# Performance work log

Hardware: AMD Instinct MI355X
Metric: run time of the kernel (lower is better)

## Reference

```python
import jax, jax.numpy as jnp
import numpy as np

B, T, D_MODEL, N_HEADS = 2, 2048, 4096, 32
D_HEAD = D_MODEL // N_HEADS
ROPE_THETA = 20000.0


def _rope_tables(seq_len, d_head, theta):
    # Faithful to RotaryEmbedding + apply_rotary_emb's `[..., ::2]` slicing:
    # emb = concat(freqs, freqs) along feature dim, then every-other element taken.
    inv_freq = 1.0 / (theta ** (jnp.arange(0, d_head, 2, dtype=jnp.float32) / d_head))  # [d/2]
    t = jnp.arange(seq_len, dtype=jnp.float32)
    freqs = jnp.einsum('i,j->ij', t, inv_freq)          # [T, d/2]
    emb = jnp.concatenate([freqs, freqs], axis=-1)       # [T, d]
    cos_h = jnp.cos(emb)[:, ::2]                         # [T, d/2]
    sin_h = jnp.sin(emb)[:, ::2]                         # [T, d/2]
    return cos_h, sin_h


def _apply_rope(x, cos_h, sin_h):
    # x: [B, H, T, d]; pairs are interleaved (even/odd feature indices).
    x1 = x[..., 0::2]
    x2 = x[..., 1::2]
    r1 = x1 * cos_h - x2 * sin_h
    r2 = x1 * sin_h + x2 * cos_h
    return jnp.stack((r1, r2), axis=-1).reshape(x.shape)


def setup_inputs() -> dict:
    key = jax.random.key(0)
    kx, kq, kk, kv, ko = jax.random.split(key, 5)
    s = 0.02
    return {
        'hidden_states': jax.random.normal(kx, (B, T, D_MODEL), dtype=jnp.float32),
        'Wq': jax.random.normal(kq, (D_MODEL, D_MODEL), dtype=jnp.float32) * s,
        'Wk': jax.random.normal(kk, (D_MODEL, D_MODEL), dtype=jnp.float32) * s,
        'Wv': jax.random.normal(kv, (D_MODEL, D_MODEL), dtype=jnp.float32) * s,
        'Wo': jax.random.normal(ko, (D_MODEL, D_MODEL), dtype=jnp.float32) * s,
    }


def reference(hidden_states, Wq, Wk, Wv, Wo):
    Bs, Ts, C = hidden_states.shape
    H, Dh = N_HEADS, C // N_HEADS

    # QKV projections (nn.Linear: y = x @ W.T), split heads -> [B, H, T, Dh]
    def proj(W):
        return (hidden_states @ W.T).reshape(Bs, Ts, H, Dh).transpose(0, 2, 1, 3)

    q, k, v = proj(Wq), proj(Wk), proj(Wv)

    cos_h, sin_h = _rope_tables(Ts, Dh, ROPE_THETA)
    q = _apply_rope(q, cos_h, sin_h)
    k = _apply_rope(k, cos_h, sin_h)

    # Causal scaled-dot-product attention (flash path semantics)
    scale = 1.0 / jnp.sqrt(jnp.asarray(Dh, dtype=q.dtype))
    scores = jnp.einsum('bhqd,bhkd->bhqk', q, k) * scale      # [B,H,T,T]
    causal = jnp.tril(jnp.ones((Ts, Ts), dtype=bool))
    scores = jnp.where(causal, scores, jnp.finfo(scores.dtype).min)
    probs = jax.nn.softmax(scores, axis=-1)
    attn = jnp.einsum('bhqk,bhkd->bhqd', probs, v)            # [B,H,T,Dh]

    attn = attn.transpose(0, 2, 1, 3).reshape(Bs, Ts, C)
    return attn @ Wo.T
```

## Files before the change

kernel.cpp:

```cpp
#include <hip/hip_runtime.h>
#include <hip/hip_bf16.h>


typedef __bf16 bf16x8 __attribute__((ext_vector_type(8)));
typedef __bf16 bf16x4 __attribute__((ext_vector_type(4)));
typedef float  f32x4  __attribute__((ext_vector_type(4)));

#define GLD_A1(p) ((__attribute__((address_space(1))) void*)(p))
#define GLD_A3(p) ((__attribute__((address_space(3))) void*)(p))

static constexpr int   BATCH = 2;
static constexpr int   TSEQ  = 2048;
static constexpr int   DM    = 4096;
static constexpr int   NH    = 32;
static constexpr int   DH    = 128;
static constexpr size_t TS   = (size_t)DM * DM;

__global__ __launch_bounds__(256) void cast_f32_bf16(const float* __restrict__ in,
                                                     __bf16* __restrict__ out) {
    size_t id = (size_t)blockIdx.x * blockDim.x + threadIdx.x;
    float4 v = ((const float4*)in)[id];
    bf16x4 o = { (__bf16)v.x, (__bf16)v.y, (__bf16)v.z, (__bf16)v.w };
    *(bf16x4*)(out + id * 4) = o;
}

template <bool OUT_F32>
__global__ __launch_bounds__(256) void gemm_nt(const __bf16* __restrict__ A,
                                               const __bf16* __restrict__ W,
                                               void* __restrict__ Cout) {
    constexpr int Kd = 4096, Nd = 4096;
    __shared__ alignas(16) __bf16 As[128 * 32];
    __shared__ alignas(16) __bf16 Bs[128 * 32];

    const int t = threadIdx.x, w = t >> 6, L = t & 63;
    const int lane15 = L & 15, quad = L >> 4;
    const int rowBlock = blockIdx.y * 128, colBlock = blockIdx.x * 128;
    const int wr = (w >> 1) * 64, wc = (w & 1) * 64;

    f32x4 acc[4][4] = {};

    for (int kb = 0; kb < Kd; kb += 32) {
        __syncthreads();
#pragma unroll
        for (int i = 0; i < 2; i++) {
            const int chunk = w * 128 + i * 64 + L;
            const int row = chunk >> 2, c8 = (chunk & 3) * 8;
            __builtin_amdgcn_global_load_lds(
                GLD_A1(A + (size_t)(rowBlock + row) * Kd + kb + c8),
                GLD_A3(As + (size_t)(w * 128 + i * 64) * 8), 16, 0, 0);
            __builtin_amdgcn_global_load_lds(
                GLD_A1(W + (size_t)(colBlock + row) * Kd + kb + c8),
                GLD_A3(Bs + (size_t)(w * 128 + i * 64) * 8), 16, 0, 0);
        }
        __syncthreads();

        bf16x8 a[4], b[4];
#pragma unroll
        for (int i = 0; i < 4; i++)
            a[i] = *(const bf16x8*)(As + (wr + i * 16 + lane15) * 32 + quad * 8);
#pragma unroll
        for (int j = 0; j < 4; j++)
            b[j] = *(const bf16x8*)(Bs + (wc + j * 16 + lane15) * 32 + quad * 8);
#pragma unroll
        for (int i = 0; i < 4; i++)
#pragma unroll
            for (int j = 0; j < 4; j++)
                acc[i][j] = __builtin_amdgcn_mfma_f32_16x16x32_bf16(a[i], b[j], acc[i][j], 0, 0, 0);
    }

#pragma unroll
    for (int i = 0; i < 4; i++)
#pragma unroll
        for (int j = 0; j < 4; j++)
#pragma unroll
            for (int r = 0; r < 4; r++) {
                const size_t gm = rowBlock + wr + i * 16 + quad * 4 + r;
                const size_t gn = colBlock + wc + j * 16 + lane15;
                if (OUT_F32)
                    ((float*)Cout)[gm * Nd + gn] = acc[i][j][r];
                else
                    ((__bf16*)Cout)[gm * Nd + gn] = (__bf16)acc[i][j][r];
            }
}

__global__ __launch_bounds__(256) void rope_inplace(__bf16* __restrict__ X) {
    const size_t id = (size_t)blockIdx.x * blockDim.x + threadIdx.x;
    const int g = (int)(id & 511);
    const size_t row = id >> 9;
    const int tpos = (int)(row & (TSEQ - 1));
    __bf16* p = X + row * DM + (size_t)g * 8;
    bf16x8 v = *(const bf16x8*)p;
    bf16x8 o;
#pragma unroll
    for (int pr = 0; pr < 4; pr++) {
        const int pcol = g * 4 + pr;
        const int j = (2 * (pcol & 63)) & 63;
        const float inv = exp2f(-(float)j * (14.287712379549449f / 64.0f));
        const float ang = (float)tpos * inv;
        float s, c;
        sincosf(ang, &s, &c);
        const float x0 = (float)v[2 * pr], x1 = (float)v[2 * pr + 1];
        o[2 * pr]     = (__bf16)(x0 * c - x1 * s);
        o[2 * pr + 1] = (__bf16)(x0 * s + x1 * c);
    }
    *(bf16x8*)p = o;
}

__global__ __launch_bounds__(256) void flash_attn(const __bf16* __restrict__ Qg,
                                                  const __bf16* __restrict__ Kg,
                                                  const __bf16* __restrict__ Vg,
                                                  __bf16* __restrict__ Og) {
    const int qb = blockIdx.x;
    const int bh = blockIdx.y;
    const int b = bh >> 5, h = bh & 31;
    const size_t base = (size_t)b * TSEQ * DM + (size_t)h * DH;
    const __bf16* Qp = Qg + base;
    const __bf16* Kp = Kg + base;
    const __bf16* Vp = Vg + base;
    __bf16*       Op = Og + base;

    __shared__ alignas(16) __bf16 Ks[64 * 128];
    __shared__ alignas(16) __bf16 Vt[128 * 64];
    __shared__ alignas(16) __bf16 Ps[64 * 72];

    const int t = threadIdx.x, w = t >> 6, L = t & 63;
    const int lane15 = L & 15, quad = L >> 4;
    const int sw = (lane15 & 7) << 4;

    bf16x8 aq[4];
    {
        const int qrow = qb * 64 + w * 16 + lane15;
#pragma unroll
        for (int ks = 0; ks < 4; ++ks)
            aq[ks] = *(const bf16x8*)(Qp + (size_t)qrow * DM + ks * 32 + quad * 8);
    }

    f32x4 o[8] = {};
    float m_i[4], l_i[4];
#pragma unroll
    for (int r = 0; r < 4; r++) { m_i[r] = -1e30f; l_i[r] = 0.0f; }
    const float scale = 0.08838834764831845f;

    for (int kt = 0; kt <= qb; ++kt) {
        bf16x8 vv[4];
#pragma unroll
        for (int c = 0; c < 4; c++) {
            const int d0 = (c * 4 + w) * 8;
            vv[c] = *(const bf16x8*)(Vp + (size_t)(kt * 64 + L) * DM + d0);
        }
#pragma unroll
        for (int c = 0; c < 4; c++) {
            const int chunk0 = c * 256 + (w << 6);
            const int chunk  = chunk0 + L;
            const int row = chunk >> 4;
            const int ssw = (chunk & 15) ^ (row & 7);
            __builtin_amdgcn_global_load_lds(
                GLD_A1(Kp + (size_t)(kt * 64 + row) * DM + ssw * 8),
                GLD_A3((char*)Ks + chunk0 * 16), 16, 0, 0);
        }
#pragma unroll
        for (int c = 0; c < 4; c++) {
            const int d0 = (c * 4 + w) * 8;
#pragma unroll
            for (int jj = 0; jj < 8; jj++)
                *(__bf16*)((char*)Vt + (d0 + jj) * 128 + ((L * 2) ^ (jj << 4))) = vv[c][jj];
        }
        __syncthreads();

        f32x4 s[4] = {};
        __builtin_amdgcn_s_setprio(1);
#pragma unroll
        for (int ks = 0; ks < 4; ++ks)
#pragma unroll
            for (int n = 0; n < 4; n++) {
                bf16x8 bk = *(const bf16x8*)((const char*)Ks + (n * 16 + lane15) * 256
                                             + ((ks * 64 + quad * 16) ^ sw));
                s[n] = __builtin_amdgcn_mfma_f32_16x16x32_bf16(aq[ks], bk, s[n], 0, 0, 0);
            }
        __builtin_amdgcn_s_setprio(0);

        const bool diag = (kt == qb);
#pragma unroll
        for (int n = 0; n < 4; n++) {
            const int col = kt * 64 + n * 16 + lane15;
#pragma unroll
            for (int r = 0; r < 4; r++) {
                const int rowq = qb * 64 + w * 16 + quad * 4 + r;
                float sv = s[n][r] * scale;
                if (diag && col > rowq) sv = -1e30f;
                s[n][r] = sv;
            }
        }

        float mx[4], al[4], rs[4];
#pragma unroll
        for (int r = 0; r < 4; r++)
            mx[r] = fmaxf(fmaxf(s[0][r], s[1][r]), fmaxf(s[2][r], s[3][r]));
#pragma unroll
        for (int off = 8; off >= 1; off >>= 1)
#pragma unroll
            for (int r = 0; r < 4; r++)
                mx[r] = fmaxf(mx[r], __shfl_xor(mx[r], off));
#pragma unroll
        for (int r = 0; r < 4; r++) {
            const float mn = fmaxf(m_i[r], mx[r]);
            al[r] = __expf(m_i[r] - mn);
            m_i[r] = mn;
            rs[r] = 0.0f;
        }
#pragma unroll
        for (int n = 0; n < 4; n++)
#pragma unroll
            for (int r = 0; r < 4; r++) {
                const float p = __expf(s[n][r] - m_i[r]);
                rs[r] += p;
                Ps[(w * 16 + quad * 4 + r) * 72 + n * 16 + lane15] = (__bf16)p;
            }
#pragma unroll
        for (int off = 8; off >= 1; off >>= 1)
#pragma unroll
            for (int r = 0; r < 4; r++)
                rs[r] += __shfl_xor(rs[r], off);
#pragma unroll
        for (int r = 0; r < 4; r++) l_i[r] = l_i[r] * al[r] + rs[r];
#pragma unroll
        for (int d = 0; d < 8; ++d)
#pragma unroll
            for (int r = 0; r < 4; r++) o[d][r] *= al[r];

        __syncthreads();

        __builtin_amdgcn_s_setprio(1);
#pragma unroll
        for (int ks2 = 0; ks2 < 2; ++ks2) {
            bf16x8 ap = *(const bf16x8*)(Ps + (w * 16 + lane15) * 72 + ks2 * 32 + quad * 8);
#pragma unroll
            for (int d = 0; d < 8; ++d) {
                bf16x8 bv = *(const bf16x8*)((const char*)Vt + (d * 16 + lane15) * 128
                                             + ((ks2 * 64 + quad * 16) ^ sw));
                o[d] = __builtin_amdgcn_mfma_f32_16x16x32_bf16(ap, bv, o[d], 0, 0, 0);
            }
        }
        __builtin_amdgcn_s_setprio(0);
        __syncthreads();
    }

    float inv_l[4];
#pragma unroll
    for (int r = 0; r < 4; r++) inv_l[r] = 1.0f / l_i[r];
#pragma unroll
    for (int d = 0; d < 8; ++d)
#pragma unroll
        for (int r = 0; r < 4; r++) {
            const int rowq = qb * 64 + w * 16 + quad * 4 + r;
            Op[(size_t)rowq * DM + d * 16 + lane15] = (__bf16)(o[d][r] * inv_l[r]);
        }
}

extern "C" void kernel_launch(void* const* d_in, const int* in_sizes, int n_in,
                              void* d_out, int out_size, void* d_ws, size_t ws_size,
                              hipStream_t stream) {
    const float* hs = (const float*)d_in[0];
    const float* Wq = (const float*)d_in[1];
    const float* Wk = (const float*)d_in[2];
    const float* Wv = (const float*)d_in[3];
    const float* Wo = (const float*)d_in[4];
    float* out = (float*)d_out;

    __bf16* hs_b = (__bf16*)d_ws;
    __bf16* wq_b = hs_b + TS;
    __bf16* wk_b = wq_b + TS;
    __bf16* wv_b = wk_b + TS;
    __bf16* wo_b = wv_b + TS;
    __bf16* Qb   = wo_b + TS;
    __bf16* Kb   = Qb + TS;
    __bf16* Vb   = Kb + TS;
    __bf16* Ab   = Vb + TS;
    if (ws_size < 9 * TS * sizeof(__bf16)) return;

    const dim3 blk(256);
    const int castGrid = (int)(TS / 4 / 256);
    cast_f32_bf16<<<castGrid, blk, 0, stream>>>(hs, hs_b);
    cast_f32_bf16<<<castGrid, blk, 0, stream>>>(Wq, wq_b);
    cast_f32_bf16<<<castGrid, blk, 0, stream>>>(Wk, wk_b);
    cast_f32_bf16<<<castGrid, blk, 0, stream>>>(Wv, wv_b);
    cast_f32_bf16<<<castGrid, blk, 0, stream>>>(Wo, wo_b);

    const dim3 ggrid(32, 32);
    gemm_nt<false><<<ggrid, blk, 0, stream>>>(hs_b, wq_b, (void*)Qb);
    gemm_nt<false><<<ggrid, blk, 0, stream>>>(hs_b, wk_b, (void*)Kb);
    gemm_nt<false><<<ggrid, blk, 0, stream>>>(hs_b, wv_b, (void*)Vb);

    const int ropeGrid = (int)(TS / 8 / 256);
    rope_inplace<<<ropeGrid, blk, 0, stream>>>(Qb);
    rope_inplace<<<ropeGrid, blk, 0, stream>>>(Kb);

    flash_attn<<<dim3(32, 64), blk, 0, stream>>>(Qb, Kb, Vb, Ab);

    gemm_nt<true><<<ggrid, blk, 0, stream>>>(Ab, wo_b, (void*)out);
}
```

Baseline: 1.507 ms.

## Transpose flash-attention S layout, reverse block order, and batch cast/rope launches

```diff
diff --git a/kernel.cpp b/kernel.cpp
--- a/kernel.cpp
+++ b/kernel.cpp
@@ -4,6 +4,7 @@
 
 typedef __bf16 bf16x8 __attribute__((ext_vector_type(8)));
 typedef __bf16 bf16x4 __attribute__((ext_vector_type(4)));
+typedef __bf16 bf16x2 __attribute__((ext_vector_type(2)));
 typedef float  f32x4  __attribute__((ext_vector_type(4)));
 
 #define GLD_A1(p) ((__attribute__((address_space(1))) void*)(p))
@@ -16,12 +17,19 @@
 static constexpr int   DH    = 128;
 static constexpr size_t TS   = (size_t)DM * DM;
 
-__global__ __launch_bounds__(256) void cast_f32_bf16(const float* __restrict__ in,
-                                                     __bf16* __restrict__ out) {
+__global__ __launch_bounds__(256) void cast5_f32_bf16(const float* __restrict__ s0,
+                                                      const float* __restrict__ s1,
+                                                      const float* __restrict__ s2,
+                                                      const float* __restrict__ s3,
+                                                      const float* __restrict__ s4,
+                                                      __bf16* __restrict__ out) {
+    const int which = blockIdx.y;
+    const float* s = which == 0 ? s0 : which == 1 ? s1 : which == 2 ? s2
+                   : which == 3 ? s3 : s4;
     size_t id = (size_t)blockIdx.x * blockDim.x + threadIdx.x;
-    float4 v = ((const float4*)in)[id];
+    float4 v = ((const float4*)s)[id];
     bf16x4 o = { (__bf16)v.x, (__bf16)v.y, (__bf16)v.z, (__bf16)v.w };
-    *(bf16x4*)(out + id * 4) = o;
+    *(bf16x4*)(out + (size_t)which * TS + id * 4) = o;
 }
 
 template <bool OUT_F32>
@@ -83,7 +91,9 @@
             }
 }
 
-__global__ __launch_bounds__(256) void rope_inplace(__bf16* __restrict__ X) {
+__global__ __launch_bounds__(256) void rope2_inplace(__bf16* __restrict__ Q,
+                                                     __bf16* __restrict__ K) {
+    __bf16* X = blockIdx.y == 0 ? Q : K;
     const size_t id = (size_t)blockIdx.x * blockDim.x + threadIdx.x;
     const int g = (int)(id & 511);
     const size_t row = id >> 9;
@@ -110,7 +120,7 @@
                                                   const __bf16* __restrict__ Kg,
                                                   const __bf16* __restrict__ Vg,
                                                   __bf16* __restrict__ Og) {
-    const int qb = blockIdx.x;
+    const int qb = 31 - blockIdx.x;
     const int bh = blockIdx.y;
     const int b = bh >> 5, h = bh & 31;
     const size_t base = (size_t)b * TSEQ * DM + (size_t)h * DH;
@@ -121,27 +131,26 @@
 
     __shared__ alignas(16) __bf16 Ks[64 * 128];
     __shared__ alignas(16) __bf16 Vt[128 * 64];
-    __shared__ alignas(16) __bf16 Ps[64 * 72];
+    __shared__ alignas(16) __bf16 Ps[64 * 64];
 
     const int t = threadIdx.x, w = t >> 6, L = t & 63;
     const int lane15 = L & 15, quad = L >> 4;
     const int sw = (lane15 & 7) << 4;
-
-    bf16x8 aq[4];
-    {
-        const int qrow = qb * 64 + w * 16 + lane15;
-#pragma unroll
-        for (int ks = 0; ks < 4; ++ks)
-            aq[ks] = *(const bf16x8*)(Qp + (size_t)qrow * DM + ks * 32 + quad * 8);
-    }
+    const int rowPs = w * 16 + lane15;
+
+    bf16x8 bq[4];
+    const int qrow = qb * 64 + w * 16 + lane15;
+#pragma unroll
+    for (int ks = 0; ks < 4; ++ks)
+        bq[ks] = *(const bf16x8*)(Qp + (size_t)qrow * DM + ks * 32 + quad * 8);
 
     f32x4 o[8] = {};
-    float m_i[4], l_i[4];
-#pragma unroll
-    for (int r = 0; r < 4; r++) { m_i[r] = -1e30f; l_i[r] = 0.0f; }
+    float m_i = -1e30f, l_i = 0.0f;
     const float scale = 0.08838834764831845f;
 
     for (int kt = 0; kt <= qb; ++kt) {
+        if (kt) __syncthreads();
+
         bf16x8 vv[4];
 #pragma unroll
         for (int c = 0; c < 4; c++) {
@@ -173,67 +182,72 @@
         for (int ks = 0; ks < 4; ++ks)
 #pragma unroll
             for (int n = 0; n < 4; n++) {
-                bf16x8 bk = *(const bf16x8*)((const char*)Ks + (n * 16 + lane15) * 256
+                bf16x8 ak = *(const bf16x8*)((const char*)Ks + (n * 16 + lane15) * 256
                                              + ((ks * 64 + quad * 16) ^ sw));
-                s[n] = __builtin_amdgcn_mfma_f32_16x16x32_bf16(aq[ks], bk, s[n], 0, 0, 0);
+                s[n] = __builtin_amdgcn_mfma_f32_16x16x32_bf16(ak, bq[ks], s[n], 0, 0, 0);
             }
         __builtin_amdgcn_s_setprio(0);
 
         const bool diag = (kt == qb);
 #pragma unroll
-        for (int n = 0; n < 4; n++) {
-            const int col = kt * 64 + n * 16 + lane15;
+        for (int n = 0; n < 4; n++)
 #pragma unroll
             for (int r = 0; r < 4; r++) {
-                const int rowq = qb * 64 + w * 16 + quad * 4 + r;
+                const int col = kt * 64 + n * 16 + quad * 4 + r;
                 float sv = s[n][r] * scale;
-                if (diag && col > rowq) sv = -1e30f;
+                if (diag && col > qrow) sv = -1e30f;
                 s[n][r] = sv;
             }
-        }
-
-        float mx[4], al[4], rs[4];
-#pragma unroll
-        for (int r = 0; r < 4; r++)
-            mx[r] = fmaxf(fmaxf(s[0][r], s[1][r]), fmaxf(s[2][r], s[3][r]));
-#pragma unroll
-        for (int off = 8; off >= 1; off >>= 1)
-#pragma unroll
-            for (int r = 0; r < 4; r++)
-                mx[r] = fmaxf(mx[r], __shfl_xor(mx[r], off));
-#pragma unroll
-        for (int r = 0; r < 4; r++) {
-            const float mn = fmaxf(m_i[r], mx[r]);
-            al[r] = __expf(m_i[r] - mn);
-            m_i[r] = mn;
-            rs[r] = 0.0f;
-        }
+
+        float mx = s[0][0];
 #pragma unroll
         for (int n = 0; n < 4; n++)
 #pragma unroll
+            for (int r = 0; r < 4; r++) mx = fmaxf(mx, s[n][r]);
+        mx = fmaxf(mx, __shfl_xor(mx, 16));
+        mx = fmaxf(mx, __shfl_xor(mx, 32));
+        const float mn = fmaxf(m_i, mx);
+        const float al = __expf(m_i - mn);
+        m_i = mn;
+
+        float p[4][4];
+        float rs = 0.0f;
+#pragma unroll
+        for (int n = 0; n < 4; n++)
+#pragma unroll
             for (int r = 0; r < 4; r++) {
-                const float p = __expf(s[n][r] - m_i[r]);
-                rs[r] += p;
-                Ps[(w * 16 + quad * 4 + r) * 72 + n * 16 + lane15] = (__bf16)p;
-            }
-#pragma unroll
-        for (int off = 8; off >= 1; off >>= 1)
-#pragma unroll
-            for (int r = 0; r < 4; r++)
-                rs[r] += __shfl_xor(rs[r], off);
-#pragma unroll
-        for (int r = 0; r < 4; r++) l_i[r] = l_i[r] * al[r] + rs[r];
+                p[n][r] = __expf(s[n][r] - mn);
+                rs += p[n][r];
+            }
+        rs += __shfl_xor(rs, 16);
+        rs += __shfl_xor(rs, 32);
+        l_i = l_i * al + rs;
+
+#pragma unroll
+        for (int n = 0; n < 4; n++)
+#pragma unroll
+            for (int hh = 0; hh < 2; hh++) {
+                bf16x2 pr = { (__bf16)p[n][2 * hh], (__bf16)p[n][2 * hh + 1] };
+                const int byte = rowPs * 128 + ((n * 32 + quad * 8 + hh * 4) ^ sw);
+                *(bf16x2*)((char*)Ps + byte) = pr;
+            }
+
+        float alr[4];
+#pragma unroll
+        for (int r = 0; r < 4; r++) alr[r] = __shfl(al, quad * 4 + r);
 #pragma unroll
         for (int d = 0; d < 8; ++d)
 #pragma unroll
-            for (int r = 0; r < 4; r++) o[d][r] *= al[r];
-
-        __syncthreads();
+            for (int r = 0; r < 4; r++) o[d][r] *= alr[r];
+
+        asm volatile("s_waitcnt lgkmcnt(0)" ::: "memory");
+        __builtin_amdgcn_sched_barrier(0);
 
         __builtin_amdgcn_s_setprio(1);
 #pragma unroll
         for (int ks2 = 0; ks2 < 2; ++ks2) {
-            bf16x8 ap = *(const bf16x8*)(Ps + (w * 16 + lane15) * 72 + ks2 * 32 + quad * 8);
+            bf16x8 ap = *(const bf16x8*)((const char*)Ps + rowPs * 128
+                                         + ((ks2 * 64 + quad * 16) ^ sw));
 #pragma unroll
             for (int d = 0; d < 8; ++d) {
                 bf16x8 bv = *(const bf16x8*)((const char*)Vt + (d * 16 + lane15) * 128
@@ -242,18 +256,17 @@
             }
         }
         __builtin_amdgcn_s_setprio(0);
-        __syncthreads();
     }
 
-    float inv_l[4];
-#pragma unroll
-    for (int r = 0; r < 4; r++) inv_l[r] = 1.0f / l_i[r];
+    float lr[4];
+#pragma unroll
+    for (int r = 0; r < 4; r++) lr[r] = 1.0f / __shfl(l_i, quad * 4 + r);
 #pragma unroll
     for (int d = 0; d < 8; ++d)
 #pragma unroll
         for (int r = 0; r < 4; r++) {
             const int rowq = qb * 64 + w * 16 + quad * 4 + r;
-            Op[(size_t)rowq * DM + d * 16 + lane15] = (__bf16)(o[d][r] * inv_l[r]);
+            Op[(size_t)rowq * DM + d * 16 + lane15] = (__bf16)(o[d][r] * lr[r]);
         }
 }
 
@@ -279,21 +292,14 @@
     if (ws_size < 9 * TS * sizeof(__bf16)) return;
 
     const dim3 blk(256);
-    const int castGrid = (int)(TS / 4 / 256);
-    cast_f32_bf16<<<castGrid, blk, 0, stream>>>(hs, hs_b);
-    cast_f32_bf16<<<castGrid, blk, 0, stream>>>(Wq, wq_b);
-    cast_f32_bf16<<<castGrid, blk, 0, stream>>>(Wk, wk_b);
-    cast_f32_bf16<<<castGrid, blk, 0, stream>>>(Wv, wv_b);
-    cast_f32_bf16<<<castGrid, blk, 0, stream>>>(Wo, wo_b);
+    cast5_f32_bf16<<<dim3(TS / 4 / 256, 5), blk, 0, stream>>>(hs, Wq, Wk, Wv, Wo, hs_b);
 
     const dim3 ggrid(32, 32);
     gemm_nt<false><<<ggrid, blk, 0, stream>>>(hs_b, wq_b, (void*)Qb);
     gemm_nt<false><<<ggrid, blk, 0, stream>>>(hs_b, wk_b, (void*)Kb);
     gemm_nt<false><<<ggrid, blk, 0, stream>>>(hs_b, wv_b, (void*)Vb);
 
-    const int ropeGrid = (int)(TS / 8 / 256);
-    rope_inplace<<<ropeGrid, blk, 0, stream>>>(Qb);
-    rope_inplace<<<ropeGrid, blk, 0, stream>>>(Kb);
+    rope2_inplace<<<dim3(TS / 8 / 256, 2), blk, 0, stream>>>(Qb, Kb);
 
     flash_attn<<<dim3(32, 64), blk, 0, stream>>>(Qb, Kb, Vb, Ab);
 
```

After: 1.361 ms. 1.11x faster.
